# Performance work log

Measured on AMD Instinct MI355X. Metric: run time of the kernel, lower is better.

## Reference

```python
import jax, jax.numpy as jnp
import numpy as np

NEG_SLOP = 0.2
N_NODES, N_EDGES, IN_FT, HID, N_LAYERS = 50000, 800000, 256, 128, 3


def setup_inputs() -> dict:
    key = jax.random.key(0)
    ks = jax.random.split(key, 8)
    x = jax.random.normal(ks[0], (N_NODES, IN_FT), jnp.float32)
    edge_index = jax.random.randint(ks[1], (2, N_EDGES), 0, N_NODES, jnp.int32)
    edge_weight = jax.random.uniform(ks[2], (N_EDGES,), jnp.float32)
    # learned params: input projection + per-layer GATConv params (heads=1)
    Wlin = jax.random.normal(ks[3], (IN_FT, HID), jnp.float32) / np.float32(np.sqrt(IN_FT))
    blin = jnp.zeros((HID,), jnp.float32)
    Wc = jax.random.normal(ks[4], (N_LAYERS, HID, HID), jnp.float32) / np.float32(np.sqrt(HID))
    att_src = jax.random.normal(ks[5], (N_LAYERS, HID), jnp.float32) * 0.1
    att_dst = jax.random.normal(ks[6], (N_LAYERS, HID), jnp.float32) * 0.1
    bias_c = jnp.zeros((N_LAYERS, HID), jnp.float32)
    return {"x": x, "edge_index": edge_index, "edge_weight": edge_weight,
            "numNode": N_NODES, "Wlin": Wlin, "blin": blin, "Wc": Wc,
            "att_src": att_src, "att_dst": att_dst, "bias_c": bias_c}


def _gat_conv(h, src, dst, ew, W, a_src, a_dst, b, n):
    # single-head GATConv (add_self_loops=False, concat=False)
    hp = h @ W                                   # [N, H]
    logit = jax.nn.leaky_relu((hp @ a_src)[src] + (hp @ a_dst)[dst], NEG_SLOP)  # [E]
    m = jax.ops.segment_max(logit, dst, num_segments=n)
    m = jnp.where(jnp.isfinite(m), m, 0.0)       # empty segments -> -inf guard
    e = jnp.exp(logit - m[dst]) * ew             # edge_weight scales attention
    denom = jax.ops.segment_sum(e, dst, num_segments=n)
    alpha = e / (denom[dst] + 1e-16)             # scatter-softmax over in-edges
    return jax.ops.segment_sum(hp[src] * alpha[:, None], dst, num_segments=n) + b


def reference(x, edge_index, edge_weight, numNode, Wlin, blin, Wc, att_src, att_dst, bias_c):
    n = x.shape[0]
    src, dst = edge_index[0], edge_index[1]
    h = x @ Wlin + blin                          # input projection
    n_layers = Wc.shape[0]
    layers_ret = []
    for i in range(n_layers):
        tmp = _gat_conv(h, src, dst, edge_weight, Wc[i], att_src[i], att_dst[i], bias_c[i], n)
        if i < n_layers - 1:
            h = h + tmp                          # residual; dropout = identity (eval)
            layers_ret.append(h[:numNode])
        else:
            layers_ret.append(tmp[:numNode])
    # update='max': elementwise max over layer outputs
    return jnp.max(jnp.stack(layers_ret, axis=0), axis=0)
```

## Files before the change

### kernel.cpp

```cpp
#include <hip/hip_runtime.h>
#include <cstdint>
#include <cstddef>

#define NN 50000
#define NE 800000
#define FIN 256
#define HD 128
#define NEG_SLOPE 0.2f

#define NBK 196
#define NCH 98
#define NCHP 104
#define CHUNK 8192

typedef short s16x8 __attribute__((ext_vector_type(8)));
typedef float f32x4 __attribute__((ext_vector_type(4)));

__device__ inline ushort f2bf(float f) {
    uint32_t u = __float_as_uint(f);
    u += 0x7FFFu + ((u >> 16) & 1u);
    return (ushort)(u >> 16);
}
__device__ inline float bf2f(ushort h) {
    return __uint_as_float(((uint32_t)h) << 16);
}


__global__ __launch_bounds__(1024) void k_bhist(const int* __restrict__ dst,
                                                int* __restrict__ bhist) {
    __shared__ int hist[NBK];
    const int tid = threadIdx.x, blk = blockIdx.x;
    if (tid < NBK) hist[tid] = 0;
    __syncthreads();
    const int e0 = blk * CHUNK;
    #pragma unroll
    for (int u = 0; u < CHUNK / 1024; ++u) {
        int e = e0 + u * 1024 + tid;
        if (e < NE) atomicAdd(&hist[dst[e] >> 8], 1);
    }
    __syncthreads();
    if (tid < NBK) {
        bhist[tid * NCHP + blk] = hist[tid];
        if (blk == 0)
            for (int c = NCH; c < NCHP; ++c) bhist[tid * NCHP + c] = 0;
    }
}

__global__ __launch_bounds__(256) void k_bscan(int* __restrict__ bhist,
                                               int* __restrict__ bbeg,
                                               int* __restrict__ row_ptr) {
    __shared__ int wsum[4];
    const int tid = threadIdx.x;
    int4 buf[NCHP / 4];
    int tot = 0;
    if (tid < NBK) {
        const int4* rp = reinterpret_cast<const int4*>(bhist + tid * NCHP);
        #pragma unroll
        for (int u = 0; u < NCHP / 4; ++u) buf[u] = rp[u];
        #pragma unroll
        for (int u = 0; u < NCHP / 4; ++u) {
            int4 v = buf[u], o;
            o.x = tot; tot += v.x;
            o.y = tot; tot += v.y;
            o.z = tot; tot += v.z;
            o.w = tot; tot += v.w;
            buf[u] = o;
        }
    }
    const int lane = tid & 63, wid = tid >> 6;
    int x = tot;
    #pragma unroll
    for (int o = 1; o < 64; o <<= 1) {
        int t = __shfl_up(x, o);
        if (lane >= o) x += t;
    }
    if (lane == 63) wsum[wid] = x;
    __syncthreads();
    int wo = 0;
    for (int k = 0; k < wid; ++k) wo += wsum[k];
    const int excl = x - tot + wo;
    if (tid < NBK) {
        bbeg[tid] = excl;
        int4* rp = reinterpret_cast<int4*>(bhist + tid * NCHP);
        #pragma unroll
        for (int u = 0; u < NCHP / 4; ++u) {
            int4 v = buf[u];
            v.x += excl; v.y += excl; v.z += excl; v.w += excl;
            rp[u] = v;
        }
    }
    if (tid == 0) { bbeg[NBK] = NE; row_ptr[NN] = NE; }
}

__global__ __launch_bounds__(1024) void k_binscatter(const int* __restrict__ src,
                                                     const int* __restrict__ dst,
                                                     const float* __restrict__ ew,
                                                     const int* __restrict__ bhist,
                                                     uint2* __restrict__ epk) {
    __shared__ int base[NBK];
    __shared__ int lcur[NBK];
    const int tid = threadIdx.x, blk = blockIdx.x;
    if (tid < NBK) { base[tid] = bhist[tid * NCHP + blk]; lcur[tid] = 0; }
    __syncthreads();
    const int e0 = blk * CHUNK;
    #pragma unroll
    for (int u = 0; u < CHUNK / 1024; ++u) {
        int e = e0 + u * 1024 + tid;
        if (e < NE) {
            int d = dst[e];
            int s = src[e];
            float w = ew[e];
            int b = d >> 8;
            int pos = base[b] + atomicAdd(&lcur[b], 1);
            epk[pos] = make_uint2((uint32_t)s | ((uint32_t)(d & 255) << 16),
                                  __float_as_uint(w));
        }
    }
}

__global__ __launch_bounds__(256) void k_build(const uint2* __restrict__ epk,
                                               const int* __restrict__ bbeg,
                                               int* __restrict__ row_ptr,
                                               unsigned int* __restrict__ cw) {
    __shared__ int cnt[256];
    __shared__ int cur[256];
    __shared__ int wsum[4];
    const int tid = threadIdx.x, b = blockIdx.x;
    const int n0 = b << 8;
    const int ebeg = bbeg[b], eend = bbeg[b + 1];
    cnt[tid] = 0;
    __syncthreads();
    for (int e = ebeg + tid; e < eend; e += 256)
        atomicAdd(&cnt[(epk[e].x >> 16) & 255], 1);
    __syncthreads();
    const int v = cnt[tid];
    const int lane = tid & 63, wid = tid >> 6;
    int x = v;
    #pragma unroll
    for (int o = 1; o < 64; o <<= 1) {
        int t = __shfl_up(x, o);
        if (lane >= o) x += t;
    }
    if (lane == 63) wsum[wid] = x;
    __syncthreads();
    int wo = 0;
    for (int k = 0; k < wid; ++k) wo += wsum[k];
    const int excl = ebeg + x - v + wo;
    if (n0 + tid < NN) row_ptr[n0 + tid] = excl;
    cur[tid] = excl;
    __syncthreads();
    for (int e = ebeg + tid; e < eend; e += 256) {
        uint2 p = epk[e];
        int dl = (p.x >> 16) & 255;
        int pos = atomicAdd(&cur[dl], 1);
        cw[pos] = (p.x & 0xFFFFu) |
                  ((unsigned int)f2bf(__uint_as_float(p.y)) << 16);
    }
}


__global__ void k_split_all(const float* __restrict__ Wlin,
                            const float* __restrict__ Wc,
                            ushort* __restrict__ Th, ushort* __restrict__ Tl) {
    int idx = blockIdx.x * blockDim.x + threadIdx.x;
    const int NLIN = HD * FIN;
    float f;
    if (idx < NLIN) {
        int n = idx / FIN, k = idx - n * FIN;
        f = Wlin[(size_t)k * HD + n];
    } else if (idx < NLIN + 3 * HD * HD) {
        int r = idx - NLIN;
        int l = r / (HD * HD);
        int rr = r - l * (HD * HD);
        int n = rr / HD, k = rr - n * HD;
        f = Wc[(size_t)l * HD * HD + (size_t)k * HD + n];
    } else return;
    ushort hi = f2bf(f);
    Th[idx] = hi;
    Tl[idx] = f2bf(f - bf2f(hi));
}


template <int K, bool ATT, bool ABF16, bool OUT8, bool WLO>
__global__ __launch_bounds__(256) void k_gemm_mfma(
    const float*  __restrict__ Af,
    const ushort* __restrict__ Ab,
    const ushort* __restrict__ Bh,
    const ushort* __restrict__ Bl,
    const float*  __restrict__ bias,
    ushort*       __restrict__ Cb,
    unsigned char* __restrict__ C8,
    const float*  __restrict__ att_s, const float* __restrict__ att_d,
    float2* __restrict__ asig,
    float*  __restrict__ ad_,
    int M)
{
    constexpr int BK = 128;
    constexpr int NT = K / BK;
    __shared__ ushort Bs[WLO ? 32768 : 16384];

    const int tid  = threadIdx.x;
    const int lane = tid & 63;
    const int wid  = tid >> 6;
    const int fl   = lane & 15;
    const int fg   = lane >> 4;
    const int rowBase = blockIdx.x * 128 + wid * 32;

    f32x4 acc[2][8] = {};

    for (int t = 0; t < NT; ++t) {
        if (t) __syncthreads();
        #pragma unroll
        for (int u = 0; u < 8; ++u) {
            const int id  = u * 256 + tid;
            const int bcol = id >> 4, c = id & 15;
            const size_t g = (size_t)bcol * K + t * BK + c * 8;
            const int lidx = bcol * 128 + ((c ^ (bcol & 15)) << 3);
            *reinterpret_cast<uint4*>(&Bs[lidx]) =
                *reinterpret_cast<const uint4*>(Bh + g);
            if (WLO)
                *reinterpret_cast<uint4*>(&Bs[16384 + lidx]) =
                    *reinterpret_cast<const uint4*>(Bl + g);
        }
        __syncthreads();

        #pragma unroll
        for (int kt = 0; kt < BK / 32; ++kt) {
            s16x8 a_h[2], a_l[2];
            #pragma unroll
            for (int rt = 0; rt < 2; ++rt) {
                int r = rowBase + rt * 16 + fl;
                if (r >= M) r = M - 1;
                if (ABF16) {
                    a_h[rt] = *reinterpret_cast<const s16x8*>(
                        Ab + (size_t)r * K + t * BK + kt * 32 + fg * 8);
                } else {
                    const float* ap = Af + (size_t)r * K + t * BK + kt * 32 + fg * 8;
                    float4 t0 = *reinterpret_cast<const float4*>(ap);
                    float4 t1 = *reinterpret_cast<const float4*>(ap + 4);
                    float v[8] = {t0.x, t0.y, t0.z, t0.w, t1.x, t1.y, t1.z, t1.w};
                    #pragma unroll
                    for (int u = 0; u < 8; ++u) {
                        ushort h0 = f2bf(v[u]);
                        a_h[rt][u] = (short)h0;
                        a_l[rt][u] = (short)f2bf(v[u] - bf2f(h0));
                    }
                }
            }
            #pragma unroll
            for (int ct = 0; ct < 8; ++ct) {
                const int lidx = (ct * 16 + fl) * 128 + (((kt * 4 + fg) ^ fl) << 3);
                s16x8 b_h = *reinterpret_cast<const s16x8*>(&Bs[lidx]);
                #pragma unroll
                for (int rt = 0; rt < 2; ++rt) {
                    acc[rt][ct] = __builtin_amdgcn_mfma_f32_16x16x32_bf16(a_h[rt], b_h, acc[rt][ct], 0, 0, 0);
                    if (WLO) {
                        s16x8 b_l = *reinterpret_cast<const s16x8*>(&Bs[16384 + lidx]);
                        acc[rt][ct] = __builtin_amdgcn_mfma_f32_16x16x32_bf16(a_h[rt], b_l, acc[rt][ct], 0, 0, 0);
                    }
                    if (!ABF16)
                        acc[rt][ct] = __builtin_amdgcn_mfma_f32_16x16x32_bf16(a_l[rt], b_h, acc[rt][ct], 0, 0, 0);
                }
            }
        }
    }

    float bval[8];
    #pragma unroll
    for (int ct = 0; ct < 8; ++ct) bval[ct] = bias ? bias[ct * 16 + fl] : 0.f;
    float asv[8], adv[8];
    if (ATT) {
        #pragma unroll
        for (int ct = 0; ct < 8; ++ct) {
            asv[ct] = att_s[ct * 16 + fl];
            adv[ct] = att_d[ct * 16 + fl];
        }
    }

    #pragma unroll
    for (int rt = 0; rt < 2; ++rt) {
        const int rbase = rowBase + rt * 16 + fg * 4;
        #pragma unroll
        for (int r = 0; r < 4; ++r) {
            const int row = rbase + r;
            const bool ok = row < M;
            float sv = 0.f, dv = 0.f, m = 0.f;
            float val[8];
            #pragma unroll
            for (int ct = 0; ct < 8; ++ct) {
                val[ct] = acc[rt][ct][r] + bval[ct];
                if (ATT) { sv = fmaf(val[ct], asv[ct], sv); dv = fmaf(val[ct], adv[ct], dv); }
                if (OUT8) m = fmaxf(m, fabsf(val[ct]));
            }
            if (OUT8) {
                #pragma unroll
                for (int o = 1; o < 16; o <<= 1) m = fmaxf(m, __shfl_xor(m, o));
                const float qs = 127.f / fmaxf(m, 1e-30f);
                #pragma unroll
                for (int ct = 0; ct < 8; ++ct) {
                    int qv = (int)rintf(val[ct] * qs);
                    qv = qv < -127 ? -127 : (qv > 127 ? 127 : qv);
                    if (ok) C8[(size_t)row * HD + ct * 16 + fl] =
                        (unsigned char)(qv + 128);
                }
            } else {
                #pragma unroll
                for (int ct = 0; ct < 8; ++ct)
                    if (ok) Cb[(size_t)row * HD + ct * 16 + fl] = f2bf(val[ct]);
            }
            if (ATT) {
                #pragma unroll
                for (int o = 1; o < 16; o <<= 1) {
                    sv += __shfl_xor(sv, o);
                    dv += __shfl_xor(dv, o);
                }
                if (fl == 0 && ok) {
                    asig[row] = make_float2(sv, OUT8 ? m * (1.f / 127.f) : 0.f);
                    ad_[row]  = dv;
                }
            }
        }
    }
}


__device__ inline void acc8u(float wj, uint2 pv,
                             float& a0, float& a1, float& a2, float& a3,
                             float& a4, float& a5, float& a6, float& a7) {
    a0 = fmaf(wj, (float)( pv.x        & 0xFFu), a0);
    a1 = fmaf(wj, (float)((pv.x >>  8) & 0xFFu), a1);
    a2 = fmaf(wj, (float)((pv.x >> 16) & 0xFFu), a2);
    a3 = fmaf(wj, (float)( pv.x >> 24         ), a3);
    a4 = fmaf(wj, (float)( pv.y        & 0xFFu), a4);
    a5 = fmaf(wj, (float)((pv.y >>  8) & 0xFFu), a5);
    a6 = fmaf(wj, (float)((pv.y >> 16) & 0xFFu), a6);
    a7 = fmaf(wj, (float)( pv.y >> 24         ), a7);
}

__global__ __launch_bounds__(256) void k_agg(const unsigned char* __restrict__ hp8,
                                             const float2* __restrict__ asig,
                                             ushort* __restrict__ hb,
                                             const float* __restrict__ ad_,
                                             const int* __restrict__ row_ptr,
                                             const unsigned int* __restrict__ cw,
                                             const float* __restrict__ bias,
                                             float* __restrict__ out,
                                             ushort* __restrict__ mx, int mode) {
    __shared__ uint2 swb[4][64];
    const int wid  = threadIdx.x >> 6;
    const int lane = threadIdx.x & 63;
    const int g    = lane >> 4;
    const int hl   = lane & 15;
    const int d    = blockIdx.x * 16 + wid * 4 + g;
    const int beg = row_ptr[d], end = row_ptr[d + 1];
    const float adv = ad_[d];
    const int hlo = hl << 3;
    const int sb  = g << 4;

    float a0 = 0.f, a1 = 0.f, a2 = 0.f, a3 = 0.f;
    float a4 = 0.f, a5 = 0.f, a6 = 0.f, a7 = 0.f;
    float dloc = 0.f, wesum = 0.f;

    for (int base = beg; base < end; base += 16) {
        const int n = min(16, end - base);
        unsigned soff = 0; float w = 0.f, we = 0.f;
        if (hl < n) {
            unsigned int v = cw[base + hl];
            unsigned s = v & 0xFFFFu;
            float2 ag = asig[s];
            float l = ag.x + adv;
            l = (l >= 0.f) ? l : NEG_SLOPE * l;
            l = fminf(l, 80.f);
            w  = __expf(l) * bf2f((ushort)(v >> 16));
            we = w * ag.y;
            soff = s << 7;
        }
        dloc += w;
        swb[wid][sb + hl] = make_uint2(soff, __float_as_uint(we));

        const int nr = (n > 8) ? 16 : 8;
        for (int i = 0; i < nr; i += 8) {
            uint2 sw[8]; uint2 pv[8];
            #pragma unroll
            for (int j = 0; j < 8; ++j)
                sw[j] = swb[wid][sb + i + j];
            #pragma unroll
            for (int j = 0; j < 8; ++j)
                pv[j] = *reinterpret_cast<const uint2*>(hp8 + sw[j].x + hlo);
            #pragma unroll
            for (int j = 0; j < 8; ++j) {
                const float wj = __uint_as_float(sw[j].y);
                acc8u(wj, pv[j], a0, a1, a2, a3, a4, a5, a6, a7);
                wesum += wj;
            }
        }
    }
    #pragma unroll
    for (int o = 1; o < 16; o <<= 1) dloc += __shfl_xor(dloc, o);

    const float c = 128.f * wesum;
    const float inv = 1.f / (dloc + 1e-16f);
    const int f0 = hl * 8;
    float r0 = (a0 - c) * inv + bias[f0 + 0], r1 = (a1 - c) * inv + bias[f0 + 1];
    float r2 = (a2 - c) * inv + bias[f0 + 2], r3 = (a3 - c) * inv + bias[f0 + 3];
    float r4 = (a4 - c) * inv + bias[f0 + 4], r5 = (a5 - c) * inv + bias[f0 + 5];
    float r6 = (a6 - c) * inv + bias[f0 + 6], r7 = (a7 - c) * inv + bias[f0 + 7];

    if (mode == 2) {
        uint4 mv = *reinterpret_cast<const uint4*>(mx + (size_t)d * HD + f0);
        f32x4 o0, o1;
        o0[0] = fmaxf(bf2f((ushort)mv.x),         r0);
        o0[1] = fmaxf(bf2f((ushort)(mv.x >> 16)), r1);
        o0[2] = fmaxf(bf2f((ushort)mv.y),         r2);
        o0[3] = fmaxf(bf2f((ushort)(mv.y >> 16)), r3);
        o1[0] = fmaxf(bf2f((ushort)mv.z),         r4);
        o1[1] = fmaxf(bf2f((ushort)(mv.z >> 16)), r5);
        o1[2] = fmaxf(bf2f((ushort)mv.w),         r6);
        o1[3] = fmaxf(bf2f((ushort)(mv.w >> 16)), r7);
        f32x4* outp = reinterpret_cast<f32x4*>(out + (size_t)d * HD + f0);
        __builtin_nontemporal_store(o0, outp);
        __builtin_nontemporal_store(o1, outp + 1);
    } else {
        uint4* hp = reinterpret_cast<uint4*>(hb + (size_t)d * HD + f0);
        uint4 hv = *hp;
        float h0 = bf2f((ushort)hv.x), h1 = bf2f((ushort)(hv.x >> 16));
        float h2 = bf2f((ushort)hv.y), h3 = bf2f((ushort)(hv.y >> 16));
        float h4 = bf2f((ushort)hv.z), h5 = bf2f((ushort)(hv.z >> 16));
        float h6 = bf2f((ushort)hv.w), h7 = bf2f((ushort)(hv.w >> 16));
        float n0 = h0 + r0, n1 = h1 + r1, n2 = h2 + r2, n3 = h3 + r3;
        float n4 = h4 + r4, n5 = h5 + r5, n6 = h6 + r6, n7 = h7 + r7;
        uint4 st;
        st.x = (uint32_t)f2bf(n0) | ((uint32_t)f2bf(n1) << 16);
        st.y = (uint32_t)f2bf(n2) | ((uint32_t)f2bf(n3) << 16);
        st.z = (uint32_t)f2bf(n4) | ((uint32_t)f2bf(n5) << 16);
        st.w = (uint32_t)f2bf(n6) | ((uint32_t)f2bf(n7) << 16);
        *hp = st;
        if (mode == 1) {
            uint4 sm;
            sm.x = (uint32_t)f2bf(fmaxf(h0, n0)) | ((uint32_t)f2bf(fmaxf(h1, n1)) << 16);
            sm.y = (uint32_t)f2bf(fmaxf(h2, n2)) | ((uint32_t)f2bf(fmaxf(h3, n3)) << 16);
            sm.z = (uint32_t)f2bf(fmaxf(h4, n4)) | ((uint32_t)f2bf(fmaxf(h5, n5)) << 16);
            sm.w = (uint32_t)f2bf(fmaxf(h6, n6)) | ((uint32_t)f2bf(fmaxf(h7, n7)) << 16);
            *reinterpret_cast<uint4*>(mx + (size_t)d * HD + f0) = sm;
        }
    }
}


extern "C" void kernel_launch(void* const* d_in, const int* in_sizes, int n_in,
                              void* d_out, int out_size, void* d_ws, size_t ws_size,
                              hipStream_t stream) {
    const float* x        = (const float*)d_in[0];
    const int*   ei       = (const int*)d_in[1];
    const float* ew       = (const float*)d_in[2];
    const float* Wlin     = (const float*)d_in[4];
    const float* blin     = (const float*)d_in[5];
    const float* Wc       = (const float*)d_in[6];
    const float* att_src  = (const float*)d_in[7];
    const float* att_dst  = (const float*)d_in[8];
    const float* bias_c   = (const float*)d_in[9];
    float* out = (float*)d_out;

    const int* src = ei;
    const int* dst = ei + NE;

    char* w = (char*)d_ws;
    ushort* hb      = (ushort*)w;  w += (size_t)NN * HD * 2;
    unsigned char* hp8 = (unsigned char*)w; w += (size_t)NN * HD;
    float2* asig    = (float2*)w;  w += (size_t)NN * 8;
    ushort* mx      = (ushort*)w;  w += (size_t)NN * HD * 2;
    float*  ad_     = (float*)w;   w += (size_t)NN * 4;
    int*    row_ptr = (int*)w;     w += (size_t)(NN + 4) * 4;
    unsigned int* cw = (unsigned int*)w; w += (size_t)NE * 4;
    uint2*  epk     = (uint2*)w;   w += (size_t)NE * 8;
    int*    bhist   = (int*)w;     w += (size_t)NBK * NCHP * 4;
    int*    bbeg    = (int*)w;     w += (size_t)(NBK + 4) * 4;
    ushort* WTh     = (ushort*)w;  w += (size_t)(HD * FIN + 3 * HD * HD) * 2;
    ushort* WTl     = (ushort*)w;  w += (size_t)(HD * FIN + 3 * HD * HD) * 2;
    ushort* WlinTh = WTh,            *WlinTl = WTl;
    ushort* WcTh   = WTh + HD * FIN, *WcTl   = WTl + HD * FIN;

    const int TB = 256;
    const int nblk_w = NN / 16;
    const int nblk_g = (NN + 127) / 128;
    const int nsplit = HD * FIN + 3 * HD * HD;

    k_split_all<<<(nsplit + TB - 1) / TB, TB, 0, stream>>>(Wlin, Wc, WTh, WTl);

    k_bhist<<<NCH, 1024, 0, stream>>>(dst, bhist);
    k_bscan<<<1, 256, 0, stream>>>(bhist, bbeg, row_ptr);
    k_binscatter<<<NCH, 1024, 0, stream>>>(src, dst, ew, bhist, epk);
    k_build<<<NBK, 256, 0, stream>>>(epk, bbeg, row_ptr, cw);

    k_gemm_mfma<FIN, false, false, false, true><<<nblk_g, TB, 0, stream>>>(
        x, nullptr, WlinTh, WlinTl, blin, hb, nullptr,
        nullptr, nullptr, nullptr, nullptr, NN);

    for (int layer = 0; layer < 3; ++layer) {
        k_gemm_mfma<HD, true, true, true, false><<<nblk_g, TB, 0, stream>>>(
            nullptr, hb, WcTh + (size_t)layer * HD * HD, nullptr,
            nullptr, nullptr, hp8,
            att_src + layer * HD, att_dst + layer * HD, asig, ad_, NN);
        int mode = (layer == 0) ? 0 : (layer == 2 ? 2 : 1);
        k_agg<<<nblk_w, TB, 0, stream>>>(hp8, asig, hb, ad_, row_ptr, cw,
                                         bias_c + layer * HD, out, mx, mode);
    }
}
```

Measured before the change: 170.3 us.

## Merge preprocessing kernels: fuse histogram with weight split, projection GEMM with scatter

```diff
diff --git a/kernel.cpp b/kernel.cpp
--- a/kernel.cpp
+++ b/kernel.cpp
@@ -12,6 +12,9 @@
 #define NCH 98
 #define NCHP 104
 #define CHUNK 8192
+#define NSPLIT (HD * FIN + 3 * HD * HD)
+#define NSB 80
+#define NGP 391
 
 typedef short s16x8 __attribute__((ext_vector_type(8)));
 typedef float f32x4 __attribute__((ext_vector_type(4)));
@@ -26,23 +29,48 @@
 }
 
 
-__global__ __launch_bounds__(1024) void k_bhist(const int* __restrict__ dst,
-                                                int* __restrict__ bhist) {
+__global__ __launch_bounds__(1024) void k_pre(const int* __restrict__ dst,
+                                              int* __restrict__ bhist,
+                                              const float* __restrict__ Wlin,
+                                              const float* __restrict__ Wc,
+                                              ushort* __restrict__ Th,
+                                              ushort* __restrict__ Tl) {
     __shared__ int hist[NBK];
-    const int tid = threadIdx.x, blk = blockIdx.x;
-    if (tid < NBK) hist[tid] = 0;
-    __syncthreads();
-    const int e0 = blk * CHUNK;
-    #pragma unroll
-    for (int u = 0; u < CHUNK / 1024; ++u) {
-        int e = e0 + u * 1024 + tid;
-        if (e < NE) atomicAdd(&hist[dst[e] >> 8], 1);
-    }
-    __syncthreads();
-    if (tid < NBK) {
-        bhist[tid * NCHP + blk] = hist[tid];
-        if (blk == 0)
-            for (int c = NCH; c < NCHP; ++c) bhist[tid * NCHP + c] = 0;
+    const int tid = threadIdx.x;
+    if (blockIdx.x < NCH) {
+        const int blk = blockIdx.x;
+        if (tid < NBK) hist[tid] = 0;
+        __syncthreads();
+        const int e0 = blk * CHUNK;
+        #pragma unroll
+        for (int u = 0; u < CHUNK / 1024; ++u) {
+            int e = e0 + u * 1024 + tid;
+            if (e < NE) atomicAdd(&hist[dst[e] >> 8], 1);
+        }
+        __syncthreads();
+        if (tid < NBK) {
+            bhist[tid * NCHP + blk] = hist[tid];
+            if (blk == 0)
+                for (int c = NCH; c < NCHP; ++c) bhist[tid * NCHP + c] = 0;
+        }
+    } else {
+        int idx = (blockIdx.x - NCH) * 1024 + tid;
+        if (idx >= NSPLIT) return;
+        const int NLIN = HD * FIN;
+        float f;
+        if (idx < NLIN) {
+            int n = idx / FIN, k = idx - n * FIN;
+            f = Wlin[(size_t)k * HD + n];
+        } else {
+            int r = idx - NLIN;
+            int l = r / (HD * HD);
+            int rr = r - l * (HD * HD);
+            int n = rr / HD, k = rr - n * HD;
+            f = Wc[(size_t)l * HD * HD + (size_t)k * HD + n];
+        }
+        ushort hi = f2bf(f);
+        Th[idx] = hi;
+        Tl[idx] = f2bf(f - bf2f(hi));
     }
 }
 
@@ -92,28 +120,115 @@
     if (tid == 0) { bbeg[NBK] = NE; row_ptr[NN] = NE; }
 }
 
-__global__ __launch_bounds__(1024) void k_binscatter(const int* __restrict__ src,
-                                                     const int* __restrict__ dst,
-                                                     const float* __restrict__ ew,
-                                                     const int* __restrict__ bhist,
-                                                     uint2* __restrict__ epk) {
-    __shared__ int base[NBK];
-    __shared__ int lcur[NBK];
-    const int tid = threadIdx.x, blk = blockIdx.x;
-    if (tid < NBK) { base[tid] = bhist[tid * NCHP + blk]; lcur[tid] = 0; }
-    __syncthreads();
-    const int e0 = blk * CHUNK;
-    #pragma unroll
-    for (int u = 0; u < CHUNK / 1024; ++u) {
-        int e = e0 + u * 1024 + tid;
-        if (e < NE) {
-            int d = dst[e];
-            int s = src[e];
-            float w = ew[e];
-            int b = d >> 8;
-            int pos = base[b] + atomicAdd(&lcur[b], 1);
-            epk[pos] = make_uint2((uint32_t)s | ((uint32_t)(d & 255) << 16),
-                                  __float_as_uint(w));
+
+__global__ __launch_bounds__(256) void k_gemmproj_scatter(
+    const float*  __restrict__ x,
+    const ushort* __restrict__ Bh,
+    const ushort* __restrict__ Bl,
+    const float*  __restrict__ bias,
+    ushort*       __restrict__ Cb,
+    const int*    __restrict__ src,
+    const int*    __restrict__ dst,
+    const float*  __restrict__ ew,
+    const int*    __restrict__ bhist,
+    uint2*        __restrict__ epk,
+    int M)
+{
+    __shared__ ushort Bs[32768];
+    const int tid = threadIdx.x;
+
+    if (blockIdx.x < NGP) {
+        constexpr int K = FIN, BK = 128;
+        const int lane = tid & 63;
+        const int wid  = tid >> 6;
+        const int fl   = lane & 15;
+        const int fg   = lane >> 4;
+        const int rowBase = blockIdx.x * 128 + wid * 32;
+
+        f32x4 acc[2][8] = {};
+
+        for (int t = 0; t < K / BK; ++t) {
+            if (t) __syncthreads();
+            #pragma unroll
+            for (int u = 0; u < 8; ++u) {
+                const int id  = u * 256 + tid;
+                const int bcol = id >> 4, c = id & 15;
+                const size_t g = (size_t)bcol * K + t * BK + c * 8;
+                const int lidx = bcol * 128 + ((c ^ (bcol & 15)) << 3);
+                *reinterpret_cast<uint4*>(&Bs[lidx]) =
+                    *reinterpret_cast<const uint4*>(Bh + g);
+                *reinterpret_cast<uint4*>(&Bs[16384 + lidx]) =
+                    *reinterpret_cast<const uint4*>(Bl + g);
+            }
+            __syncthreads();
+
+            #pragma unroll
+            for (int kt = 0; kt < BK / 32; ++kt) {
+                s16x8 a_h[2], a_l[2];
+                #pragma unroll
+                for (int rt = 0; rt < 2; ++rt) {
+                    int r = rowBase + rt * 16 + fl;
+                    if (r >= M) r = M - 1;
+                    const float* ap = x + (size_t)r * K + t * BK + kt * 32 + fg * 8;
+                    float4 t0 = *reinterpret_cast<const float4*>(ap);
+                    float4 t1 = *reinterpret_cast<const float4*>(ap + 4);
+                    float v[8] = {t0.x, t0.y, t0.z, t0.w, t1.x, t1.y, t1.z, t1.w};
+                    #pragma unroll
+                    for (int u = 0; u < 8; ++u) {
+                        ushort h0 = f2bf(v[u]);
+                        a_h[rt][u] = (short)h0;
+                        a_l[rt][u] = (short)f2bf(v[u] - bf2f(h0));
+                    }
+                }
+                #pragma unroll
+                for (int ct = 0; ct < 8; ++ct) {
+                    const int lidx = (ct * 16 + fl) * 128 + (((kt * 4 + fg) ^ fl) << 3);
+                    s16x8 b_h = *reinterpret_cast<const s16x8*>(&Bs[lidx]);
+                    s16x8 b_l = *reinterpret_cast<const s16x8*>(&Bs[16384 + lidx]);
+                    #pragma unroll
+                    for (int rt = 0; rt < 2; ++rt) {
+                        acc[rt][ct] = __builtin_amdgcn_mfma_f32_16x16x32_bf16(a_h[rt], b_h, acc[rt][ct], 0, 0, 0);
+                        acc[rt][ct] = __builtin_amdgcn_mfma_f32_16x16x32_bf16(a_h[rt], b_l, acc[rt][ct], 0, 0, 0);
+                        acc[rt][ct] = __builtin_amdgcn_mfma_f32_16x16x32_bf16(a_l[rt], b_h, acc[rt][ct], 0, 0, 0);
+                    }
+                }
+            }
+        }
+
+        float bval[8];
+        #pragma unroll
+        for (int ct = 0; ct < 8; ++ct) bval[ct] = bias[ct * 16 + fl];
+        #pragma unroll
+        for (int rt = 0; rt < 2; ++rt) {
+            const int rbase = rowBase + rt * 16 + fg * 4;
+            #pragma unroll
+            for (int r = 0; r < 4; ++r) {
+                const int row = rbase + r;
+                if (row >= M) continue;
+                #pragma unroll
+                for (int ct = 0; ct < 8; ++ct)
+                    Cb[(size_t)row * HD + ct * 16 + fl] = f2bf(acc[rt][ct][r] + bval[ct]);
+            }
+        }
+    } else {
+        int* base = reinterpret_cast<int*>(Bs);
+        int* lcur = reinterpret_cast<int*>(Bs) + NBK;
+        const int blk = blockIdx.x - NGP;
+        if (tid < NBK) { base[tid] = bhist[tid * NCHP + blk]; lcur[tid] = 0; }
+        __syncthreads();
+        const int e0 = blk * CHUNK;
+        #pragma unroll
+        for (int u = 0; u < CHUNK / 256; ++u) {
+            int e = e0 + u * 256 + tid;
+            if (e < NE) {
+                int d = dst[e];
+                int s = src[e];
+                float w = ew[e];
+                int b = d >> 8;
+                int pos = base[b] + atomicAdd(&lcur[b], 1);
+                epk[pos] = make_uint2((uint32_t)s | ((uint32_t)(d & 255) << 16),
+                                      __float_as_uint(w));
+            }
         }
     }
 }
@@ -159,45 +274,17 @@
 }
 
 
-__global__ void k_split_all(const float* __restrict__ Wlin,
-                            const float* __restrict__ Wc,
-                            ushort* __restrict__ Th, ushort* __restrict__ Tl) {
-    int idx = blockIdx.x * blockDim.x + threadIdx.x;
-    const int NLIN = HD * FIN;
-    float f;
-    if (idx < NLIN) {
-        int n = idx / FIN, k = idx - n * FIN;
-        f = Wlin[(size_t)k * HD + n];
-    } else if (idx < NLIN + 3 * HD * HD) {
-        int r = idx - NLIN;
-        int l = r / (HD * HD);
-        int rr = r - l * (HD * HD);
-        int n = rr / HD, k = rr - n * HD;
-        f = Wc[(size_t)l * HD * HD + (size_t)k * HD + n];
-    } else return;
-    ushort hi = f2bf(f);
-    Th[idx] = hi;
-    Tl[idx] = f2bf(f - bf2f(hi));
-}
-
-
-template <int K, bool ATT, bool ABF16, bool OUT8, bool WLO>
-__global__ __launch_bounds__(256) void k_gemm_mfma(
-    const float*  __restrict__ Af,
+__global__ __launch_bounds__(256) void k_gemm_layer(
     const ushort* __restrict__ Ab,
     const ushort* __restrict__ Bh,
-    const ushort* __restrict__ Bl,
-    const float*  __restrict__ bias,
-    ushort*       __restrict__ Cb,
     unsigned char* __restrict__ C8,
     const float*  __restrict__ att_s, const float* __restrict__ att_d,
     float2* __restrict__ asig,
     float*  __restrict__ ad_,
     int M)
 {
-    constexpr int BK = 128;
-    constexpr int NT = K / BK;
-    __shared__ ushort Bs[WLO ? 32768 : 16384];
+    constexpr int K = HD;
+    __shared__ ushort Bs[16384];
 
     const int tid  = threadIdx.x;
     const int lane = tid & 63;
@@ -208,73 +295,42 @@
 
     f32x4 acc[2][8] = {};
 
-    for (int t = 0; t < NT; ++t) {
-        if (t) __syncthreads();
-        #pragma unroll
-        for (int u = 0; u < 8; ++u) {
-            const int id  = u * 256 + tid;
-            const int bcol = id >> 4, c = id & 15;
-            const size_t g = (size_t)bcol * K + t * BK + c * 8;
-            const int lidx = bcol * 128 + ((c ^ (bcol & 15)) << 3);
-            *reinterpret_cast<uint4*>(&Bs[lidx]) =
-                *reinterpret_cast<const uint4*>(Bh + g);
-            if (WLO)
-                *reinterpret_cast<uint4*>(&Bs[16384 + lidx]) =
-                    *reinterpret_cast<const uint4*>(Bl + g);
-        }
-        __syncthreads();
-
-        #pragma unroll
-        for (int kt = 0; kt < BK / 32; ++kt) {
-            s16x8 a_h[2], a_l[2];
-            #pragma unroll
-            for (int rt = 0; rt < 2; ++rt) {
-                int r = rowBase + rt * 16 + fl;
-                if (r >= M) r = M - 1;
-                if (ABF16) {
-                    a_h[rt] = *reinterpret_cast<const s16x8*>(
-                        Ab + (size_t)r * K + t * BK + kt * 32 + fg * 8);
-                } else {
-                    const float* ap = Af + (size_t)r * K + t * BK + kt * 32 + fg * 8;
-                    float4 t0 = *reinterpret_cast<const float4*>(ap);
-                    float4 t1 = *reinterpret_cast<const float4*>(ap + 4);
-                    float v[8] = {t0.x, t0.y, t0.z, t0.w, t1.x, t1.y, t1.z, t1.w};
-                    #pragma unroll
-                    for (int u = 0; u < 8; ++u) {
-                        ushort h0 = f2bf(v[u]);
-                        a_h[rt][u] = (short)h0;
-                        a_l[rt][u] = (short)f2bf(v[u] - bf2f(h0));
-                    }
-                }
-            }
-            #pragma unroll
-            for (int ct = 0; ct < 8; ++ct) {
-                const int lidx = (ct * 16 + fl) * 128 + (((kt * 4 + fg) ^ fl) << 3);
-                s16x8 b_h = *reinterpret_cast<const s16x8*>(&Bs[lidx]);
-                #pragma unroll
-                for (int rt = 0; rt < 2; ++rt) {
-                    acc[rt][ct] = __builtin_amdgcn_mfma_f32_16x16x32_bf16(a_h[rt], b_h, acc[rt][ct], 0, 0, 0);
-                    if (WLO) {
-                        s16x8 b_l = *reinterpret_cast<const s16x8*>(&Bs[16384 + lidx]);
-                        acc[rt][ct] = __builtin_amdgcn_mfma_f32_16x16x32_bf16(a_h[rt], b_l, acc[rt][ct], 0, 0, 0);
-                    }
-                    if (!ABF16)
-                        acc[rt][ct] = __builtin_amdgcn_mfma_f32_16x16x32_bf16(a_l[rt], b_h, acc[rt][ct], 0, 0, 0);
-                }
-            }
-        }
-    }
-
-    float bval[8];
-    #pragma unroll
-    for (int ct = 0; ct < 8; ++ct) bval[ct] = bias ? bias[ct * 16 + fl] : 0.f;
+    #pragma unroll
+    for (int u = 0; u < 8; ++u) {
+        const int id  = u * 256 + tid;
+        const int bcol = id >> 4, c = id & 15;
+        const size_t g = (size_t)bcol * K + c * 8;
+        const int lidx = bcol * 128 + ((c ^ (bcol & 15)) << 3);
+        *reinterpret_cast<uint4*>(&Bs[lidx]) =
+            *reinterpret_cast<const uint4*>(Bh + g);
+    }
+    __syncthreads();
+
+    #pragma unroll
+    for (int kt = 0; kt < 4; ++kt) {
+        s16x8 a_h[2];
+        #pragma unroll
+        for (int rt = 0; rt < 2; ++rt) {
+            int r = rowBase + rt * 16 + fl;
+            if (r >= M) r = M - 1;
+            a_h[rt] = *reinterpret_cast<const s16x8*>(
+                Ab + (size_t)r * K + kt * 32 + fg * 8);
+        }
+        #pragma unroll
+        for (int ct = 0; ct < 8; ++ct) {
+            const int lidx = (ct * 16 + fl) * 128 + (((kt * 4 + fg) ^ fl) << 3);
+            s16x8 b_h = *reinterpret_cast<const s16x8*>(&Bs[lidx]);
+            #pragma unroll
+            for (int rt = 0; rt < 2; ++rt)
+                acc[rt][ct] = __builtin_amdgcn_mfma_f32_16x16x32_bf16(a_h[rt], b_h, acc[rt][ct], 0, 0, 0);
+        }
+    }
+
     float asv[8], adv[8];
-    if (ATT) {
-        #pragma unroll
-        for (int ct = 0; ct < 8; ++ct) {
-            asv[ct] = att_s[ct * 16 + fl];
-            adv[ct] = att_d[ct * 16 + fl];
-        }
+    #pragma unroll
+    for (int ct = 0; ct < 8; ++ct) {
+        asv[ct] = att_s[ct * 16 + fl];
+        adv[ct] = att_d[ct * 16 + fl];
     }
 
     #pragma unroll
@@ -288,36 +344,29 @@
             float val[8];
             #pragma unroll
             for (int ct = 0; ct < 8; ++ct) {
-                val[ct] = acc[rt][ct][r] + bval[ct];
-                if (ATT) { sv = fmaf(val[ct], asv[ct], sv); dv = fmaf(val[ct], adv[ct], dv); }
-                if (OUT8) m = fmaxf(m, fabsf(val[ct]));
-            }
-            if (OUT8) {
-                #pragma unroll
-                for (int o = 1; o < 16; o <<= 1) m = fmaxf(m, __shfl_xor(m, o));
-                const float qs = 127.f / fmaxf(m, 1e-30f);
-                #pragma unroll
-                for (int ct = 0; ct < 8; ++ct) {
-                    int qv = (int)rintf(val[ct] * qs);
-                    qv = qv < -127 ? -127 : (qv > 127 ? 127 : qv);
-                    if (ok) C8[(size_t)row * HD + ct * 16 + fl] =
-                        (unsigned char)(qv + 128);
-                }
-            } else {
-                #pragma unroll
-                for (int ct = 0; ct < 8; ++ct)
-                    if (ok) Cb[(size_t)row * HD + ct * 16 + fl] = f2bf(val[ct]);
-            }
-            if (ATT) {
-                #pragma unroll
-                for (int o = 1; o < 16; o <<= 1) {
-                    sv += __shfl_xor(sv, o);
-                    dv += __shfl_xor(dv, o);
-                }
-                if (fl == 0 && ok) {
-                    asig[row] = make_float2(sv, OUT8 ? m * (1.f / 127.f) : 0.f);
-                    ad_[row]  = dv;
-                }
+                val[ct] = acc[rt][ct][r];
+                sv = fmaf(val[ct], asv[ct], sv);
+                dv = fmaf(val[ct], adv[ct], dv);
+                m = fmaxf(m, fabsf(val[ct]));
+            }
+            #pragma unroll
+            for (int o = 1; o < 16; o <<= 1) m = fmaxf(m, __shfl_xor(m, o));
+            const float qs = 127.f / fmaxf(m, 1e-30f);
+            #pragma unroll
+            for (int ct = 0; ct < 8; ++ct) {
+                int qv = (int)rintf(val[ct] * qs);
+                qv = qv < -127 ? -127 : (qv > 127 ? 127 : qv);
+                if (ok) C8[(size_t)row * HD + ct * 16 + fl] =
+                    (unsigned char)(qv + 128);
+            }
+            #pragma unroll
+            for (int o = 1; o < 16; o <<= 1) {
+                sv += __shfl_xor(sv, o);
+                dv += __shfl_xor(dv, o);
+            }
+            if (fl == 0 && ok) {
+                asig[row] = make_float2(sv, m * (1.f / 127.f));
+                ad_[row]  = dv;
             }
         }
     }
@@ -475,31 +524,27 @@
     uint2*  epk     = (uint2*)w;   w += (size_t)NE * 8;
     int*    bhist   = (int*)w;     w += (size_t)NBK * NCHP * 4;
     int*    bbeg    = (int*)w;     w += (size_t)(NBK + 4) * 4;
-    ushort* WTh     = (ushort*)w;  w += (size_t)(HD * FIN + 3 * HD * HD) * 2;
-    ushort* WTl     = (ushort*)w;  w += (size_t)(HD * FIN + 3 * HD * HD) * 2;
+    ushort* WTh     = (ushort*)w;  w += (size_t)NSPLIT * 2;
+    ushort* WTl     = (ushort*)w;  w += (size_t)NSPLIT * 2;
     ushort* WlinTh = WTh,            *WlinTl = WTl;
-    ushort* WcTh   = WTh + HD * FIN, *WcTl   = WTl + HD * FIN;
+    ushort* WcTh   = WTh + HD * FIN;
 
     const int TB = 256;
     const int nblk_w = NN / 16;
-    const int nblk_g = (NN + 127) / 128;
-    const int nsplit = HD * FIN + 3 * HD * HD;
-
-    k_split_all<<<(nsplit + TB - 1) / TB, TB, 0, stream>>>(Wlin, Wc, WTh, WTl);
-
-    k_bhist<<<NCH, 1024, 0, stream>>>(dst, bhist);
+    const int nblk_g = NGP;
+
+    k_pre<<<NCH + NSB, 1024, 0, stream>>>(dst, bhist, Wlin, Wc, WTh, WTl);
+
     k_bscan<<<1, 256, 0, stream>>>(bhist, bbeg, row_ptr);
-    k_binscatter<<<NCH, 1024, 0, stream>>>(src, dst, ew, bhist, epk);
-    k_build<<<NBK, 256, 0, stream>>>(epk, bbeg, row_ptr, cw);
-
-    k_gemm_mfma<FIN, false, false, false, true><<<nblk_g, TB, 0, stream>>>(
-        x, nullptr, WlinTh, WlinTl, blin, hb, nullptr,
-        nullptr, nullptr, nullptr, nullptr, NN);
+
+    k_gemmproj_scatter<<<NGP + NCH, TB, 0, stream>>>(
+        x, WlinTh, WlinTl, blin, hb, src, dst, ew, bhist, epk, NN);
+
+    k_build<<<NBK, TB, 0, stream>>>(epk, bbeg, row_ptr, cw);
 
     for (int layer = 0; layer < 3; ++layer) {
-        k_gemm_mfma<HD, true, true, true, false><<<nblk_g, TB, 0, stream>>>(
-            nullptr, hb, WcTh + (size_t)layer * HD * HD, nullptr,
-            nullptr, nullptr, hp8,
+        k_gemm_layer<<<nblk_g, TB, 0, stream>>>(
+            hb, WcTh + (size_t)layer * HD * HD, hp8,
             att_src + layer * HD, att_dst + layer * HD, asig, ad_, NN);
         int mode = (layer == 0) ? 0 : (layer == 2 ? 2 : 1);
         k_agg<<<nblk_w, TB, 0, stream>>>(hp8, asig, hb, ad_, row_ptr, cw,
```

Measured after the change: 149.0 us. -12.5%, faster.
